# Kernel tuning notes

Measured on AMD Instinct MI355X. Metric: run time of the kernel, lower is better.

The kernel has to match this reference:

```python
import jax, jax.numpy as jnp
import numpy as np

B, C, D, H, W = 4, 64, 16, 32, 32
K = 1024  # num_embeddings


def setup_inputs() -> dict:
    key = jax.random.key(0)
    k1, k2 = jax.random.split(key)
    z_e = jax.random.normal(k1, (B, C, D, H, W), dtype=jnp.float32)
    embedding = jax.random.normal(k2, (K, C), dtype=jnp.float32)
    return {"z_e": z_e, "embedding": embedding}


def reference(z_e, embedding):
    Bb, Cc, Dd, Hh, Ww = z_e.shape
    # (B, D, H, W, C) -> (N, C)
    flat = jnp.transpose(z_e, (0, 2, 3, 4, 1)).reshape(-1, Cc)
    # squared-euclidean distances to codebook: [N, K]
    distances = (
        jnp.sum(flat * flat, axis=1, keepdims=True)
        - 2.0 * flat @ embedding.T
        + jnp.sum(embedding * embedding, axis=1)
    )
    encoding_indices = jnp.argmin(distances, axis=1)  # [N]
    # one_hot @ embedding == gather (same math, efficient form)
    quantized_flat = embedding[encoding_indices]  # [N, C]
    quantized = jnp.transpose(
        quantized_flat.reshape(Bb, Dd, Hh, Ww, Cc), (0, 4, 1, 2, 3)
    )
    commitment_loss = jnp.mean((jax.lax.stop_gradient(quantized) - z_e) ** 2)
    codebook_loss = jnp.mean((quantized - jax.lax.stop_gradient(z_e)) ** 2)
    # straight-through estimator
    quantized_st = z_e + jax.lax.stop_gradient(quantized - z_e)
    indices = encoding_indices.reshape(Bb, Dd, Hh, Ww)
    return quantized_st, codebook_loss, commitment_loss, indices
```

## Files before the change

### kernel.cpp

```cpp
#include <hip/hip_runtime.h>

#define NPOS    65536
#define CDIM    64
#define KCODES  1024
#define SPATIAL 16384
#define QELEMS  4194304

#define PB      64
#define NT      64
#define NTILE   16
#define XPAD    68

#define LOSS_IDX 1024

__global__ void k_norms(const float* __restrict__ emb, float* __restrict__ wsf) {
    const int k = blockIdx.x * 256 + threadIdx.x;
    if (k == 0) wsf[LOSS_IDX] = 0.0f;
    const float4* e4 = (const float4*)(emb + (size_t)k * CDIM);
    float s = 0.0f;
#pragma unroll
    for (int c = 0; c < CDIM / 4; ++c) {
        float4 e = e4[c];
        s += e.x * e.x + e.y * e.y + e.z * e.z + e.w * e.w;
    }
    wsf[k] = s;
}

#define FMA16(i, XV) \
    acc[i][0] = fmaf(XV.x, ev0.x, acc[i][0]); acc[i][1] = fmaf(XV.x, ev0.y, acc[i][1]); \
    acc[i][2] = fmaf(XV.x, ev0.z, acc[i][2]); acc[i][3] = fmaf(XV.x, ev0.w, acc[i][3]); \
    acc[i][0] = fmaf(XV.y, ev1.x, acc[i][0]); acc[i][1] = fmaf(XV.y, ev1.y, acc[i][1]); \
    acc[i][2] = fmaf(XV.y, ev1.z, acc[i][2]); acc[i][3] = fmaf(XV.y, ev1.w, acc[i][3]); \
    acc[i][0] = fmaf(XV.z, ev2.x, acc[i][0]); acc[i][1] = fmaf(XV.z, ev2.y, acc[i][1]); \
    acc[i][2] = fmaf(XV.z, ev2.z, acc[i][2]); acc[i][3] = fmaf(XV.z, ev2.w, acc[i][3]); \
    acc[i][0] = fmaf(XV.w, ev3.x, acc[i][0]); acc[i][1] = fmaf(XV.w, ev3.y, acc[i][1]); \
    acc[i][2] = fmaf(XV.w, ev3.z, acc[i][2]); acc[i][3] = fmaf(XV.w, ev3.w, acc[i][3]);

__global__ void k_fused(const float* __restrict__ z_e,
                        const float* __restrict__ emb,
                        float* __restrict__ out,
                        float* __restrict__ wsf) {
    __shared__ float X[PB][XPAD];
    __shared__ float ET[CDIM][XPAD];
    __shared__ float NRM[KCODES];
    __shared__ unsigned long long bestp[PB];

    const int t    = threadIdx.x;
    const int tx   = t & 15;
    const int ty   = t >> 4;
    const int n0   = blockIdx.x * PB;
    const int b    = n0 >> 14;
    const int dhw0 = n0 & (SPATIAL - 1);
    const float* zb = z_e + (size_t)b * (CDIM * SPATIAL) + dhw0;

#pragma unroll
    for (int i = 0; i < 16; ++i) {
        const int idx = i * 256 + t;
        const int c = idx >> 6, p = idx & 63;
        X[p][c] = zb[(size_t)c * SPATIAL + p];
    }
    *(float4*)&NRM[t * 4] = *(const float4*)(wsf + t * 4);

    const int crow  = t >> 2;
    const int cpart = (t & 3) * 16;
    float4 g0, g1, g2, g3;
    {
        const float* src = emb + (size_t)crow * CDIM + cpart;
        g0 = *(const float4*)(src + 0);  g1 = *(const float4*)(src + 4);
        g2 = *(const float4*)(src + 8);  g3 = *(const float4*)(src + 12);
    }

    unsigned long long best4[4] = {~0ull, ~0ull, ~0ull, ~0ull};

#pragma unroll 1
    for (int tile = 0; tile < NTILE; ++tile) {
        __syncthreads();
        ET[cpart +  0][crow] = g0.x; ET[cpart +  1][crow] = g0.y;
        ET[cpart +  2][crow] = g0.z; ET[cpart +  3][crow] = g0.w;
        ET[cpart +  4][crow] = g1.x; ET[cpart +  5][crow] = g1.y;
        ET[cpart +  6][crow] = g1.z; ET[cpart +  7][crow] = g1.w;
        ET[cpart +  8][crow] = g2.x; ET[cpart +  9][crow] = g2.y;
        ET[cpart + 10][crow] = g2.z; ET[cpart + 11][crow] = g2.w;
        ET[cpart + 12][crow] = g3.x; ET[cpart + 13][crow] = g3.y;
        ET[cpart + 14][crow] = g3.z; ET[cpart + 15][crow] = g3.w;
        if (tile + 1 < NTILE) {
            const float* src = emb + (size_t)((tile + 1) * NT + crow) * CDIM + cpart;
            g0 = *(const float4*)(src + 0);  g1 = *(const float4*)(src + 4);
            g2 = *(const float4*)(src + 8);  g3 = *(const float4*)(src + 12);
        }
        __syncthreads();

        float acc[4][4];
#pragma unroll
        for (int i = 0; i < 4; ++i)
#pragma unroll
            for (int j = 0; j < 4; ++j) acc[i][j] = 0.0f;

        for (int k4 = 0; k4 < 16; ++k4) {
            float4 ev0 = *(const float4*)&ET[4 * k4 + 0][4 * tx];
            float4 ev1 = *(const float4*)&ET[4 * k4 + 1][4 * tx];
            float4 ev2 = *(const float4*)&ET[4 * k4 + 2][4 * tx];
            float4 ev3 = *(const float4*)&ET[4 * k4 + 3][4 * tx];
            float4 xv0 = *(const float4*)&X[4 * ty + 0][4 * k4];
            float4 xv1 = *(const float4*)&X[4 * ty + 1][4 * k4];
            float4 xv2 = *(const float4*)&X[4 * ty + 2][4 * k4];
            float4 xv3 = *(const float4*)&X[4 * ty + 3][4 * k4];
            FMA16(0, xv0)
            FMA16(1, xv1)
            FMA16(2, xv2)
            FMA16(3, xv3)
        }

        const float4 nr = *(const float4*)&NRM[tile * NT + 4 * tx];
#pragma unroll
        for (int j = 0; j < 4; ++j) {
            const float nvj = (j == 0 ? nr.x : j == 1 ? nr.y : j == 2 ? nr.z : nr.w);
            const unsigned gk = (unsigned)(tile * NT + 4 * tx + j);
#pragma unroll
            for (int i = 0; i < 4; ++i) {
                const float s = fmaf(-2.0f, acc[i][j], nvj);
                unsigned u    = __float_as_uint(s);
                unsigned mono = (u & 0x80000000u) ? ~u : (u | 0x80000000u);
                unsigned long long pk = ((unsigned long long)mono << 10) | gk;
                if (pk < best4[i]) best4[i] = pk;
            }
        }
    }

#pragma unroll
    for (int off = 1; off < 16; off <<= 1) {
#pragma unroll
        for (int i = 0; i < 4; ++i) {
            unsigned long long o = __shfl_xor(best4[i], off, 16);
            if (o < best4[i]) best4[i] = o;
        }
    }
    if (tx == 0) {
#pragma unroll
        for (int i = 0; i < 4; ++i) bestp[4 * ty + i] = best4[i];
    }
    __syncthreads();

    const int p    = t >> 2;
    const int q4   = t & 3;
    const int bidx = (int)(bestp[p] & 1023ull);
    if (q4 == 0) out[QELEMS + 2 + n0 + p] = (float)bidx;

    float lsum = 0.0f;
    const float* eprow = emb + (size_t)bidx * CDIM + q4 * 16;
#pragma unroll
    for (int s4 = 0; s4 < 4; ++s4) {
        float4 ev = *(const float4*)(eprow + 4 * s4);
        const int c = q4 * 16 + 4 * s4;
        float4 xv = *(const float4*)&X[p][c];
        float d0 = ev.x - xv.x, d1 = ev.y - xv.y, d2 = ev.z - xv.z, d3 = ev.w - xv.w;
        *(float4*)&X[p][c] = make_float4(xv.x + d0, xv.y + d1, xv.z + d2, xv.w + d3);
        lsum = fmaf(d0, d0, lsum); lsum = fmaf(d1, d1, lsum);
        lsum = fmaf(d2, d2, lsum); lsum = fmaf(d3, d3, lsum);
    }
#pragma unroll
    for (int off = 32; off > 0; off >>= 1) lsum += __shfl_down(lsum, off, 64);
    if ((t & 63) == 0) atomicAdd(&wsf[LOSS_IDX], lsum);
    __syncthreads();

    const int pw = t & 63;
    const int cg = t >> 6;
    float* qb = out + (size_t)b * (CDIM * SPATIAL) + dhw0 + pw;
#pragma unroll
    for (int j = 0; j < 16; ++j) {
        const int c = cg + 4 * j;
        qb[(size_t)c * SPATIAL] = X[pw][c];
    }
}

__global__ void k_loss(const float* __restrict__ wsf, float* __restrict__ out) {
    const float m = wsf[LOSS_IDX] / (float)QELEMS;
    out[QELEMS]     = m;
    out[QELEMS + 1] = m;
}

extern "C" void kernel_launch(void* const* d_in, const int* in_sizes, int n_in,
                              void* d_out, int out_size, void* d_ws, size_t ws_size,
                              hipStream_t stream) {
    const float* z_e = (const float*)d_in[0];
    const float* emb = (const float*)d_in[1];
    float*       out = (float*)d_out;
    float*       wsf = (float*)d_ws;

    k_norms<<<KCODES / 256, 256, 0, stream>>>(emb, wsf);
    k_fused<<<NPOS / PB, 256, 0, stream>>>(z_e, emb, out, wsf);
    k_loss<<<1, 1, 0, stream>>>(wsf, out);
}
```

Baseline: 224.0 us.

## Enlarge register tile to 8x8 with 128x128 block tiles and swizzled LDS

Doubles the block tile to 128 positions by 128 codes, so each thread computes an 8x8 accumulator instead of 4x4. Shared-memory loads per FMA drop. Both operands are stored channel-major with a swizzled column map to avoid bank conflicts. The epilogue now gathers codebook rows directly from global memory per element and writes the output coalesced, replacing the staged transpose. The costs are higher register pressure, fewer blocks (512), and less occupancy.

Measured after the change: 258.2 us. 15.3% more time.

```diff
diff --git a/kernel.cpp b/kernel.cpp
--- a/kernel.cpp
+++ b/kernel.cpp
@@ -6,12 +6,14 @@
 #define SPATIAL 16384
 #define QELEMS  4194304
 
-#define PB      64
-#define NT      64
-#define NTILE   16
-#define XPAD    68
+#define PB      128
+#define KT      128
+#define NTILE   8
 
 #define LOSS_IDX 1024
+
+__device__ __forceinline__ int sig(int q)  { return (q >> 1) | ((q & 1) << 4); }
+__device__ __forceinline__ int xcol(int p) { return 4 * sig(p >> 2) + (p & 3); }
 
 __global__ void k_norms(const float* __restrict__ emb, float* __restrict__ wsf) {
     const int k = blockIdx.x * 256 + threadIdx.x;
@@ -26,24 +28,21 @@
     wsf[k] = s;
 }
 
-#define FMA16(i, XV) \
-    acc[i][0] = fmaf(XV.x, ev0.x, acc[i][0]); acc[i][1] = fmaf(XV.x, ev0.y, acc[i][1]); \
-    acc[i][2] = fmaf(XV.x, ev0.z, acc[i][2]); acc[i][3] = fmaf(XV.x, ev0.w, acc[i][3]); \
-    acc[i][0] = fmaf(XV.y, ev1.x, acc[i][0]); acc[i][1] = fmaf(XV.y, ev1.y, acc[i][1]); \
-    acc[i][2] = fmaf(XV.y, ev1.z, acc[i][2]); acc[i][3] = fmaf(XV.y, ev1.w, acc[i][3]); \
-    acc[i][0] = fmaf(XV.z, ev2.x, acc[i][0]); acc[i][1] = fmaf(XV.z, ev2.y, acc[i][1]); \
-    acc[i][2] = fmaf(XV.z, ev2.z, acc[i][2]); acc[i][3] = fmaf(XV.z, ev2.w, acc[i][3]); \
-    acc[i][0] = fmaf(XV.w, ev3.x, acc[i][0]); acc[i][1] = fmaf(XV.w, ev3.y, acc[i][1]); \
-    acc[i][2] = fmaf(XV.w, ev3.z, acc[i][2]); acc[i][3] = fmaf(XV.w, ev3.w, acc[i][3]);
+#define FMA_ROW(i, xs) \
+    acc[i][0] = fmaf(xs, ea.x, acc[i][0]); acc[i][1] = fmaf(xs, ea.y, acc[i][1]); \
+    acc[i][2] = fmaf(xs, ea.z, acc[i][2]); acc[i][3] = fmaf(xs, ea.w, acc[i][3]); \
+    acc[i][4] = fmaf(xs, eb.x, acc[i][4]); acc[i][5] = fmaf(xs, eb.y, acc[i][5]); \
+    acc[i][6] = fmaf(xs, eb.z, acc[i][6]); acc[i][7] = fmaf(xs, eb.w, acc[i][7]);
 
 __global__ void k_fused(const float* __restrict__ z_e,
                         const float* __restrict__ emb,
                         float* __restrict__ out,
                         float* __restrict__ wsf) {
-    __shared__ float X[PB][XPAD];
-    __shared__ float ET[CDIM][XPAD];
+    __shared__ float XT[CDIM][PB];
+    __shared__ float ET[CDIM][KT];
     __shared__ float NRM[KCODES];
     __shared__ unsigned long long bestp[PB];
+    __shared__ int bi[PB];
 
     const int t    = threadIdx.x;
     const int tx   = t & 15;
@@ -54,123 +53,127 @@
     const float* zb = z_e + (size_t)b * (CDIM * SPATIAL) + dhw0;
 
 #pragma unroll
-    for (int i = 0; i < 16; ++i) {
+    for (int i = 0; i < 32; ++i) {
         const int idx = i * 256 + t;
-        const int c = idx >> 6, p = idx & 63;
-        X[p][c] = zb[(size_t)c * SPATIAL + p];
+        const int c = idx >> 7, p = idx & 127;
+        XT[c][xcol(p)] = zb[(size_t)c * SPATIAL + p];
     }
-    *(float4*)&NRM[t * 4] = *(const float4*)(wsf + t * 4);
+    *(float4*)&NRM[4 * t] = *(const float4*)(wsf + 4 * t);
 
-    const int crow  = t >> 2;
-    const int cpart = (t & 3) * 16;
-    float4 g0, g1, g2, g3;
+    const int crow  = t & 127;
+    const int cpart = (t >> 7) << 5;
+    const int ecol  = xcol(crow);
+    float4 g0, g1, g2, g3, g4, g5, g6, g7;
     {
-        const float* src = emb + (size_t)crow * CDIM + cpart;
-        g0 = *(const float4*)(src + 0);  g1 = *(const float4*)(src + 4);
-        g2 = *(const float4*)(src + 8);  g3 = *(const float4*)(src + 12);
+        const float* es = emb + (size_t)crow * CDIM + cpart;
+        g0 = *(const float4*)(es +  0); g1 = *(const float4*)(es +  4);
+        g2 = *(const float4*)(es +  8); g3 = *(const float4*)(es + 12);
+        g4 = *(const float4*)(es + 16); g5 = *(const float4*)(es + 20);
+        g6 = *(const float4*)(es + 24); g7 = *(const float4*)(es + 28);
     }
 
-    unsigned long long best4[4] = {~0ull, ~0ull, ~0ull, ~0ull};
+    unsigned long long best8[8];
+#pragma unroll
+    for (int i = 0; i < 8; ++i) best8[i] = ~0ull;
 
 #pragma unroll 1
     for (int tile = 0; tile < NTILE; ++tile) {
         __syncthreads();
-        ET[cpart +  0][crow] = g0.x; ET[cpart +  1][crow] = g0.y;
-        ET[cpart +  2][crow] = g0.z; ET[cpart +  3][crow] = g0.w;
-        ET[cpart +  4][crow] = g1.x; ET[cpart +  5][crow] = g1.y;
-        ET[cpart +  6][crow] = g1.z; ET[cpart +  7][crow] = g1.w;
-        ET[cpart +  8][crow] = g2.x; ET[cpart +  9][crow] = g2.y;
-        ET[cpart + 10][crow] = g2.z; ET[cpart + 11][crow] = g2.w;
-        ET[cpart + 12][crow] = g3.x; ET[cpart + 13][crow] = g3.y;
-        ET[cpart + 14][crow] = g3.z; ET[cpart + 15][crow] = g3.w;
+        ET[cpart +  0][ecol] = g0.x; ET[cpart +  1][ecol] = g0.y;
+        ET[cpart +  2][ecol] = g0.z; ET[cpart +  3][ecol] = g0.w;
+        ET[cpart +  4][ecol] = g1.x; ET[cpart +  5][ecol] = g1.y;
+        ET[cpart +  6][ecol] = g1.z; ET[cpart +  7][ecol] = g1.w;
+        ET[cpart +  8][ecol] = g2.x; ET[cpart +  9][ecol] = g2.y;
+        ET[cpart + 10][ecol] = g2.z; ET[cpart + 11][ecol] = g2.w;
+        ET[cpart + 12][ecol] = g3.x; ET[cpart + 13][ecol] = g3.y;
+        ET[cpart + 14][ecol] = g3.z; ET[cpart + 15][ecol] = g3.w;
+        ET[cpart + 16][ecol] = g4.x; ET[cpart + 17][ecol] = g4.y;
+        ET[cpart + 18][ecol] = g4.z; ET[cpart + 19][ecol] = g4.w;
+        ET[cpart + 20][ecol] = g5.x; ET[cpart + 21][ecol] = g5.y;
+        ET[cpart + 22][ecol] = g5.z; ET[cpart + 23][ecol] = g5.w;
+        ET[cpart + 24][ecol] = g6.x; ET[cpart + 25][ecol] = g6.y;
+        ET[cpart + 26][ecol] = g6.z; ET[cpart + 27][ecol] = g6.w;
+        ET[cpart + 28][ecol] = g7.x; ET[cpart + 29][ecol] = g7.y;
+        ET[cpart + 30][ecol] = g7.z; ET[cpart + 31][ecol] = g7.w;
         if (tile + 1 < NTILE) {
-            const float* src = emb + (size_t)((tile + 1) * NT + crow) * CDIM + cpart;
-            g0 = *(const float4*)(src + 0);  g1 = *(const float4*)(src + 4);
-            g2 = *(const float4*)(src + 8);  g3 = *(const float4*)(src + 12);
+            const float* es = emb + (size_t)((tile + 1) * KT + crow) * CDIM + cpart;
+            g0 = *(const float4*)(es +  0); g1 = *(const float4*)(es +  4);
+            g2 = *(const float4*)(es +  8); g3 = *(const float4*)(es + 12);
+            g4 = *(const float4*)(es + 16); g5 = *(const float4*)(es + 20);
+            g6 = *(const float4*)(es + 24); g7 = *(const float4*)(es + 28);
         }
         __syncthreads();
 
-        float acc[4][4];
+        float acc[8][8];
 #pragma unroll
-        for (int i = 0; i < 4; ++i)
+        for (int i = 0; i < 8; ++i)
 #pragma unroll
-            for (int j = 0; j < 4; ++j) acc[i][j] = 0.0f;
+            for (int j = 0; j < 8; ++j) acc[i][j] = 0.0f;
 
-        for (int k4 = 0; k4 < 16; ++k4) {
-            float4 ev0 = *(const float4*)&ET[4 * k4 + 0][4 * tx];
-            float4 ev1 = *(const float4*)&ET[4 * k4 + 1][4 * tx];
-            float4 ev2 = *(const float4*)&ET[4 * k4 + 2][4 * tx];
-            float4 ev3 = *(const float4*)&ET[4 * k4 + 3][4 * tx];
-            float4 xv0 = *(const float4*)&X[4 * ty + 0][4 * k4];
-            float4 xv1 = *(const float4*)&X[4 * ty + 1][4 * k4];
-            float4 xv2 = *(const float4*)&X[4 * ty + 2][4 * k4];
-            float4 xv3 = *(const float4*)&X[4 * ty + 3][4 * k4];
-            FMA16(0, xv0)
-            FMA16(1, xv1)
-            FMA16(2, xv2)
-            FMA16(3, xv3)
+        for (int g = 0; g < 16; ++g) {
+#pragma unroll
+            for (int cj = 0; cj < 4; ++cj) {
+                const int ch = 4 * g + cj;
+                const float4 ea = *(const float4*)&ET[ch][4 * tx];
+                const float4 eb = *(const float4*)&ET[ch][4 * tx + 64];
+                const float4 xa = *(const float4*)&XT[ch][4 * ty];
+                const float4 xb = *(const float4*)&XT[ch][4 * ty + 64];
+                FMA_ROW(0, xa.x) FMA_ROW(1, xa.y) FMA_ROW(2, xa.z) FMA_ROW(3, xa.w)
+                FMA_ROW(4, xb.x) FMA_ROW(5, xb.y) FMA_ROW(6, xb.z) FMA_ROW(7, xb.w)
+            }
         }
 
-        const float4 nr = *(const float4*)&NRM[tile * NT + 4 * tx];
+        const float4 nra = *(const float4*)&NRM[tile * KT + 8 * tx];
+        const float4 nrb = *(const float4*)&NRM[tile * KT + 8 * tx + 4];
+        const float nv[8] = {nra.x, nra.y, nra.z, nra.w, nrb.x, nrb.y, nrb.z, nrb.w};
 #pragma unroll
-        for (int j = 0; j < 4; ++j) {
-            const float nvj = (j == 0 ? nr.x : j == 1 ? nr.y : j == 2 ? nr.z : nr.w);
-            const unsigned gk = (unsigned)(tile * NT + 4 * tx + j);
+        for (int j = 0; j < 8; ++j) {
+            const unsigned gk = (unsigned)(tile * KT + 8 * tx + j);
 #pragma unroll
-            for (int i = 0; i < 4; ++i) {
-                const float s = fmaf(-2.0f, acc[i][j], nvj);
+            for (int i = 0; i < 8; ++i) {
+                const float s = fmaf(-2.0f, acc[i][j], nv[j]);
                 unsigned u    = __float_as_uint(s);
                 unsigned mono = (u & 0x80000000u) ? ~u : (u | 0x80000000u);
                 unsigned long long pk = ((unsigned long long)mono << 10) | gk;
-                if (pk < best4[i]) best4[i] = pk;
+                if (pk < best8[i]) best8[i] = pk;
             }
         }
     }
 
 #pragma unroll
-    for (int off = 1; off < 16; off <<= 1) {
+    for (int off = 1; off < 16; off <<= 1)
 #pragma unroll
-        for (int i = 0; i < 4; ++i) {
-            unsigned long long o = __shfl_xor(best4[i], off, 16);
-            if (o < best4[i]) best4[i] = o;
+        for (int i = 0; i < 8; ++i) {
+            unsigned long long o = __shfl_xor(best8[i], off, 64);
+            if (o < best8[i]) best8[i] = o;
         }
-    }
-    if (tx == 0) {
+    if (tx == 0)
 #pragma unroll
-        for (int i = 0; i < 4; ++i) bestp[4 * ty + i] = best4[i];
+        for (int i = 0; i < 8; ++i) bestp[8 * ty + i] = best8[i];
+    __syncthreads();
+
+    if (t < PB) {
+        const int bx = (int)(bestp[t] & 1023ull);
+        bi[t] = bx;
+        out[QELEMS + 2 + n0 + t] = (float)bx;
     }
     __syncthreads();
 
-    const int p    = t >> 2;
-    const int q4   = t & 3;
-    const int bidx = (int)(bestp[p] & 1023ull);
-    if (q4 == 0) out[QELEMS + 2 + n0 + p] = (float)bidx;
-
     float lsum = 0.0f;
-    const float* eprow = emb + (size_t)bidx * CDIM + q4 * 16;
+    float* qb = out + (size_t)b * (CDIM * SPATIAL) + dhw0;
 #pragma unroll
-    for (int s4 = 0; s4 < 4; ++s4) {
-        float4 ev = *(const float4*)(eprow + 4 * s4);
-        const int c = q4 * 16 + 4 * s4;
-        float4 xv = *(const float4*)&X[p][c];
-        float d0 = ev.x - xv.x, d1 = ev.y - xv.y, d2 = ev.z - xv.z, d3 = ev.w - xv.w;
-        *(float4*)&X[p][c] = make_float4(xv.x + d0, xv.y + d1, xv.z + d2, xv.w + d3);
-        lsum = fmaf(d0, d0, lsum); lsum = fmaf(d1, d1, lsum);
-        lsum = fmaf(d2, d2, lsum); lsum = fmaf(d3, d3, lsum);
+    for (int i = 0; i < 32; ++i) {
+        const int idx = i * 256 + t;
+        const int c = idx >> 7, p = idx & 127;
+        const float xv = XT[c][xcol(p)];
+        const float ev = emb[(size_t)bi[p] * CDIM + c];
+        const float d  = ev - xv;
+        qb[(size_t)c * SPATIAL + p] = xv + d;
+        lsum = fmaf(d, d, lsum);
     }
 #pragma unroll
     for (int off = 32; off > 0; off >>= 1) lsum += __shfl_down(lsum, off, 64);
     if ((t & 63) == 0) atomicAdd(&wsf[LOSS_IDX], lsum);
-    __syncthreads();
-
-    const int pw = t & 63;
-    const int cg = t >> 6;
-    float* qb = out + (size_t)b * (CDIM * SPATIAL) + dhw0 + pw;
-#pragma unroll
-    for (int j = 0; j < 16; ++j) {
-        const int c = cg + 4 * j;
-        qb[(size_t)c * SPATIAL] = X[pw][c];
-    }
 }
 
 __global__ void k_loss(const float* __restrict__ wsf, float* __restrict__ out) {
```
